# Kernel tuning notes

Hardware: AMD Instinct MI355X
Metric: run time of the kernel (lower is better)

## Reference

```python
import jax, jax.numpy as jnp
import numpy as np

B, S, D, K, N = 4, 4096, 768, 24, 8192

def setup_inputs() -> dict:
    key = jax.random.key(0)
    k1, k2, k3, k4 = jax.random.split(key, 4)
    x = jax.random.normal(k1, (B, S, D), dtype=jnp.float32)
    phi = jax.random.normal(k2, (S, K), dtype=jnp.float32)
    M_inputs = jax.random.normal(k3, (D, D), dtype=jnp.float32) / np.sqrt(D)
    M_filters = jax.random.normal(k4, (K, D), dtype=jnp.float32) / np.sqrt(K)
    return {"x": x, "phi": phi, "M_inputs": M_inputs, "M_filters": M_filters, "n": N}


def reference(x, phi, M_inputs, M_filters, n):
    # STU.forward with use_approx=True, use_flash_fft=False
    bsz, sl, d = x.shape
    x_proj = x @ M_inputs               # [B, S, D]
    phi_proj = phi @ M_filters          # [S, D]
    # alternating sign sequence for the 'minus' spectral branch
    sgn = jnp.ones((1, sl, 1), dtype=x.dtype).at[:, 1::2].set(-1.0)
    # filters: [1, S, D, 1] broadcast over the plus/minus stack
    v = phi_proj[None, :, :, None]
    V = jnp.fft.rfft(v, n=n, axis=1)    # [1, n//2+1, D, 1] complex
    U = jnp.stack([x_proj, x_proj * sgn], axis=-1)  # [B, S, D, 2]
    Uf = jnp.fft.rfft(U, n=n, axis=1)   # [B, n//2+1, D, 2]
    U_conv = jnp.fft.irfft(V * Uf, n=n, axis=1)[:, :sl]  # [B, S, D, 2]
    spectral_plus = U_conv[..., 0]
    spectral_minus = U_conv[..., 1] * sgn
    return spectral_plus + spectral_minus
```

## Files before the change

kernel.cpp:

```cpp
#include <hip/hip_runtime.h>
#include <hip/hip_bf16.h>


#define NB 4
#define NS 4096
#define ND 768
#define NK 24

typedef __attribute__((ext_vector_type(8))) short short8;
typedef __attribute__((ext_vector_type(4))) float f32x4;
typedef __attribute__((ext_vector_type(4))) unsigned short u16x4;

static __device__ __forceinline__ float bf2f(unsigned short u) {
  union { unsigned int i; float f; } v; v.i = ((unsigned int)u) << 16; return v.f;
}
static __device__ __forceinline__ unsigned short f2bf(float f) {
  union { float f; unsigned int i; } v; v.f = f;
  return (unsigned short)((v.i + 0x7fffu + ((v.i >> 16) & 1u)) >> 16);
}
static __device__ __forceinline__ unsigned int f2bf2(float lo, float hi) {
  unsigned int r;
  asm("v_cvt_pk_bf16_f32 %0, %1, %2" : "=v"(r) : "v"(lo), "v"(hi));
  return r;
}

__device__ __forceinline__ float2 cadd(float2 a, float2 b){ return make_float2(a.x+b.x, a.y+b.y); }
__device__ __forceinline__ float2 csub(float2 a, float2 b){ return make_float2(a.x-b.x, a.y-b.y); }
__device__ __forceinline__ float2 cmul(float2 a, float2 b){ return make_float2(a.x*b.x-a.y*b.y, a.x*b.y+a.y*b.x); }
__device__ __forceinline__ float2 cmulc(float2 a, float2 b){ return make_float2(a.x*b.x+a.y*b.y, a.y*b.x-a.x*b.y); }

#define C4 0.70710678118654752f
#define C8 0.92387953251128674f
#define S8 0.38268343236508977f
#define TWO_PI 6.28318530717958648f

__device__ __forceinline__ void fft16_dif(float2 v[16]) {
  const float twr[8] = {1.f, C8, C4, S8, 0.f, -S8, -C4, -C8};
  const float twi[8] = {0.f, -S8, -C4, -C8, -1.f, -C8, -C4, -S8};
#pragma unroll
  for (int i = 0; i < 8; ++i) {
    float2 a = v[i], b = v[i+8];
    v[i] = cadd(a, b);
    float2 d = csub(a, b);
    v[i+8] = make_float2(d.x*twr[i]-d.y*twi[i], d.x*twi[i]+d.y*twr[i]);
  }
#pragma unroll
  for (int blk = 0; blk < 16; blk += 8)
#pragma unroll
    for (int i = 0; i < 4; ++i) {
      float2 a = v[blk+i], b = v[blk+i+4];
      v[blk+i] = cadd(a, b);
      float2 d = csub(a, b);
      v[blk+i+4] = make_float2(d.x*twr[2*i]-d.y*twi[2*i], d.x*twi[2*i]+d.y*twr[2*i]);
    }
#pragma unroll
  for (int blk = 0; blk < 16; blk += 4) {
    { float2 a = v[blk],   b = v[blk+2]; v[blk] = cadd(a,b);   v[blk+2] = csub(a,b); }
    { float2 a = v[blk+1], b = v[blk+3]; float2 d = csub(a,b);
      v[blk+1] = cadd(a,b); v[blk+3] = make_float2(d.y, -d.x); }
  }
#pragma unroll
  for (int blk = 0; blk < 16; blk += 2) {
    float2 a = v[blk], b = v[blk+1];
    v[blk] = cadd(a, b); v[blk+1] = csub(a, b);
  }
}

__device__ __forceinline__ void fft16_dif_zero8(float2 v[16]) {
  const float twr[8] = {1.f, C8, C4, S8, 0.f, -S8, -C4, -C8};
  const float twi[8] = {0.f, -S8, -C4, -C8, -1.f, -C8, -C4, -S8};
#pragma unroll
  for (int i = 1; i < 8; ++i) {
    float2 a = v[i];
    v[i+8] = make_float2(a.x*twr[i]-a.y*twi[i], a.x*twi[i]+a.y*twr[i]);
  }
  v[8] = v[0];
#pragma unroll
  for (int blk = 0; blk < 16; blk += 8)
#pragma unroll
    for (int i = 0; i < 4; ++i) {
      float2 a = v[blk+i], b = v[blk+i+4];
      v[blk+i] = cadd(a, b);
      float2 d = csub(a, b);
      v[blk+i+4] = make_float2(d.x*twr[2*i]-d.y*twi[2*i], d.x*twi[2*i]+d.y*twr[2*i]);
    }
#pragma unroll
  for (int blk = 0; blk < 16; blk += 4) {
    { float2 a = v[blk],   b = v[blk+2]; v[blk] = cadd(a,b);   v[blk+2] = csub(a,b); }
    { float2 a = v[blk+1], b = v[blk+3]; float2 d = csub(a,b);
      v[blk+1] = cadd(a,b); v[blk+3] = make_float2(d.y, -d.x); }
  }
#pragma unroll
  for (int blk = 0; blk < 16; blk += 2) {
    float2 a = v[blk], b = v[blk+1];
    v[blk] = cadd(a, b); v[blk+1] = csub(a, b);
  }
}

__device__ __forceinline__ void idft16(float2 v[16]) {
  const float twr[8] = {1.f, C8, C4, S8, 0.f, -S8, -C4, -C8};
  const float twi[8] = {0.f, S8, C4, C8, 1.f, C8, C4, S8};
#pragma unroll
  for (int blk = 0; blk < 16; blk += 2) {
    float2 a = v[blk], b = v[blk+1];
    v[blk] = cadd(a, b); v[blk+1] = csub(a, b);
  }
#pragma unroll
  for (int blk = 0; blk < 16; blk += 4) {
    { float2 a = v[blk],   b = v[blk+2]; v[blk] = cadd(a,b);   v[blk+2] = csub(a,b); }
    { float2 a = v[blk+1], b = v[blk+3]; float2 t = make_float2(-b.y, b.x);
      v[blk+1] = cadd(a,t); v[blk+3] = csub(a,t); }
  }
#pragma unroll
  for (int blk = 0; blk < 16; blk += 8)
#pragma unroll
    for (int i = 0; i < 4; ++i) {
      float2 b = v[blk+i+4];
      float2 t = make_float2(b.x*twr[2*i]-b.y*twi[2*i], b.x*twi[2*i]+b.y*twr[2*i]);
      float2 a = v[blk+i];
      v[blk+i] = cadd(a, t); v[blk+i+4] = csub(a, t);
    }
#pragma unroll
  for (int i = 0; i < 8; ++i) {
    float2 b = v[i+8];
    float2 t = make_float2(b.x*twr[i]-b.y*twi[i], b.x*twi[i]+b.y*twr[i]);
    float2 a = v[i];
    v[i] = cadd(a, t); v[i+8] = csub(a, t);
  }
}

__device__ __forceinline__ void idft16_low8(float2 v[16]) {
  const float twr[8] = {1.f, C8, C4, S8, 0.f, -S8, -C4, -C8};
  const float twi[8] = {0.f, S8, C4, C8, 1.f, C8, C4, S8};
#pragma unroll
  for (int blk = 0; blk < 16; blk += 2) {
    float2 a = v[blk], b = v[blk+1];
    v[blk] = cadd(a, b); v[blk+1] = csub(a, b);
  }
#pragma unroll
  for (int blk = 0; blk < 16; blk += 4) {
    { float2 a = v[blk],   b = v[blk+2]; v[blk] = cadd(a,b);   v[blk+2] = csub(a,b); }
    { float2 a = v[blk+1], b = v[blk+3]; float2 t = make_float2(-b.y, b.x);
      v[blk+1] = cadd(a,t); v[blk+3] = csub(a,t); }
  }
#pragma unroll
  for (int blk = 0; blk < 16; blk += 8)
#pragma unroll
    for (int i = 0; i < 4; ++i) {
      float2 b = v[blk+i+4];
      float2 t = make_float2(b.x*twr[2*i]-b.y*twi[2*i], b.x*twi[2*i]+b.y*twr[2*i]);
      float2 a = v[blk+i];
      v[blk+i] = cadd(a, t); v[blk+i+4] = csub(a, t);
    }
#pragma unroll
  for (int i = 0; i < 8; ++i) {
    float2 b = v[i+8];
    float2 t = make_float2(b.x*twr[i]-b.y*twi[i], b.x*twi[i]+b.y*twr[i]);
    v[i] = cadd(v[i], t);
  }
}

#define BR_TABLE {0,8,4,12,2,10,6,14,1,9,5,13,3,11,7,15}
#define PAD(i) ((i) + ((i) >> 4))

__global__ __launch_bounds__(256) void transpose_cast_Mi(const float* __restrict__ Mi,
                                                         unsigned short* __restrict__ MiT) {
  __shared__ float tile[64][65];
  const int d0 = blockIdx.x * 64;
  const int e0 = blockIdx.y * 64;
  const int tid = threadIdx.x;
#pragma unroll
  for (int i = 0; i < 16; ++i) {
    int ee = (tid >> 6) + i * 4;
    int dd = tid & 63;
    tile[ee][dd] = Mi[(e0 + ee) * ND + d0 + dd];
  }
  __syncthreads();
#pragma unroll
  for (int i = 0; i < 8; ++i) {
    int dd = (tid >> 5) + i * 8;
    int ee2 = (tid & 31) * 2;
    unsigned int w = f2bf2(tile[ee2][dd], tile[ee2 + 1][dd]);
    *(unsigned int*)(MiT + (size_t)(d0 + dd) * ND + e0 + ee2) = w;
  }
}

__global__ __launch_bounds__(256) void gemm_xprojT(const float* __restrict__ Xf,
                                                   const unsigned short* __restrict__ MiT,
                                                   unsigned short* __restrict__ XPT) {
  __shared__ __align__(16) unsigned char smem[33792];
  unsigned short* As0 = (unsigned short*)smem;
  unsigned short* Bs0 = As0 + 4096;
  unsigned short* As1 = Bs0 + 4096;
  unsigned short* Bs1 = As1 + 4096;

  const int tid = threadIdx.x;
  const int lane = tid & 63;
  const int wave = tid >> 6;
  const int f = blockIdx.x;
  const int swz = (f & 7) * 96 + (f >> 3);
  const int c0 = (swz % 6) * 128;
  const int r0 = (swz / 6) * 128;

  const int rowA = tid >> 2;
  const int colq = (tid & 3) * 8;

  f32x4 acc[4][4];
#pragma unroll
  for (int m = 0; m < 4; ++m)
#pragma unroll
    for (int n = 0; n < 4; ++n) acc[m][n] = (f32x4){0.f, 0.f, 0.f, 0.f};

  {
    const float* ga = Xf + (size_t)(r0 + rowA) * ND + colq;
    float4 p0 = *(const float4*)ga, p1 = *(const float4*)(ga + 4);
    const float* ga2 = ga + (size_t)64 * ND;
    float4 p2 = *(const float4*)ga2, p3 = *(const float4*)(ga2 + 4);
#pragma unroll
    for (int h = 0; h < 2; ++h) {
      int c = wave * 2 + h;
      int rowc = c * 16 + (lane >> 2);
      const unsigned short* gb = MiT + (size_t)(c0 + rowc) * ND + (lane & 3) * 8;
      __builtin_amdgcn_global_load_lds(
          (const __attribute__((address_space(1))) void*)gb,
          (__attribute__((address_space(3))) void*)(Bs0 + c * 512), 16, 0, 0);
    }
    *(uint4*)(As0 + tid * 8) = make_uint4(
        f2bf2(p0.x, p0.y), f2bf2(p0.z, p0.w), f2bf2(p1.x, p1.y), f2bf2(p1.z, p1.w));
    *(uint4*)(As0 + 2048 + tid * 8) = make_uint4(
        f2bf2(p2.x, p2.y), f2bf2(p2.z, p2.w), f2bf2(p3.x, p3.y), f2bf2(p3.z, p3.w));
  }
  __syncthreads();

  for (int t = 0; t < NK; ++t) {
    unsigned short* Ac = (t & 1) ? As1 : As0;
    unsigned short* Bc = (t & 1) ? Bs1 : Bs0;
    unsigned short* An = (t & 1) ? As0 : As1;
    unsigned short* Bn = (t & 1) ? Bs0 : Bs1;
    const bool pre = (t < NK - 1);
    float4 p0, p1, p2, p3;
    if (pre) {
      const int k0n = (t + 1) * 32;
      const float* ga = Xf + (size_t)(r0 + rowA) * ND + k0n + colq;
      p0 = *(const float4*)ga; p1 = *(const float4*)(ga + 4);
      const float* ga2 = ga + (size_t)64 * ND;
      p2 = *(const float4*)ga2; p3 = *(const float4*)(ga2 + 4);
#pragma unroll
      for (int h = 0; h < 2; ++h) {
        int c = wave * 2 + h;
        int rowc = c * 16 + (lane >> 2);
        const unsigned short* gb = MiT + (size_t)(c0 + rowc) * ND + k0n + (lane & 3) * 8;
        __builtin_amdgcn_global_load_lds(
            (const __attribute__((address_space(1))) void*)gb,
            (__attribute__((address_space(3))) void*)(Bn + c * 512), 16, 0, 0);
      }
    }

    const int wr = (wave >> 1) * 64;
    const int wc = (wave & 1) * 64;
    short8 a[4], b[4];
#pragma unroll
    for (int m = 0; m < 4; ++m)
      a[m] = *(const short8*)(Ac + (wr + m * 16 + (lane & 15)) * 32 + (lane >> 4) * 8);
#pragma unroll
    for (int n = 0; n < 4; ++n)
      b[n] = *(const short8*)(Bc + (wc + n * 16 + (lane & 15)) * 32 + (lane >> 4) * 8);
#pragma unroll
    for (int m = 0; m < 4; ++m)
#pragma unroll
      for (int n = 0; n < 4; ++n)
        acc[m][n] = __builtin_amdgcn_mfma_f32_16x16x32_bf16(a[m], b[n], acc[m][n], 0, 0, 0);

    if (pre) {
      *(uint4*)(An + tid * 8) = make_uint4(
          f2bf2(p0.x, p0.y), f2bf2(p0.z, p0.w), f2bf2(p1.x, p1.y), f2bf2(p1.z, p1.w));
      *(uint4*)(An + 2048 + tid * 8) = make_uint4(
          f2bf2(p2.x, p2.y), f2bf2(p2.z, p2.w), f2bf2(p3.x, p3.y), f2bf2(p3.z, p3.w));
      __syncthreads();
    }
  }
  __syncthreads();

  unsigned int* Cb = (unsigned int*)smem;
  const int wr = (wave >> 1) * 64;
  const int wc = (wave & 1) * 64;
#pragma unroll
  for (int m = 0; m < 4; ++m)
#pragma unroll
    for (int n = 0; n < 4; ++n) {
      int col = wc + n * 16 + (lane & 15);
      int sp = (wr + m * 16 + (lane >> 4) * 4) >> 1;
      f32x4 a4 = acc[m][n];
      *(uint2*)(Cb + col * 66 + sp) =
          make_uint2(f2bf2(a4[0], a4[1]), f2bf2(a4[2], a4[3]));
    }
  __syncthreads();
  const int bI = r0 >> 12;
  const int sBase = r0 & (NS - 1);
  {
    int col = tid >> 1, half = tid & 1;
    const unsigned int* srcl = Cb + col * 66 + half * 32;
    unsigned int* dstg = (unsigned int*)(XPT + ((size_t)bI * ND + c0 + col) * NS + sBase) + half * 32;
#pragma unroll
    for (int k = 0; k < 8; ++k)
      *(uint4*)(dstg + k * 4) = *(const uint4*)(srcl + k * 4);
  }
}

__global__ __launch_bounds__(256) void filter_fft(const float* __restrict__ phi,
                                                  const float* __restrict__ Mf,
                                                  float2* __restrict__ Hbr) {
  __shared__ float LR[4352], LI[4352];
  __shared__ float2 TA[256], TB[256];
  const int d = blockIdx.x;
  const int tid = threadIdx.x;
  const int BR[16] = BR_TABLE;
  float2 v[16];

  {
    float sn, cs;
    __sincosf(-(TWO_PI / 4096.f) * (float)tid, &sn, &cs); TA[tid] = make_float2(cs, sn);
    __sincosf(-(TWO_PI / 256.f) * (float)tid, &sn, &cs);  TB[tid] = make_float2(cs, sn);
  }

  float mf[NK];
#pragma unroll
  for (int k = 0; k < NK; ++k) mf[k] = Mf[k * ND + d];
#pragma unroll
  for (int n2 = 0; n2 < 8; ++n2) {
    int m = n2 * 256 + tid;
    const float* pr = phi + (size_t)(2 * m) * NK;
    float acc = 0.f;
#pragma unroll
    for (int k = 0; k < NK; ++k) acc += pr[k] * mf[k];
    v[n2] = make_float2(acc, 0.f);
  }
#pragma unroll
  for (int n2 = 8; n2 < 16; ++n2) v[n2] = make_float2(0.f, 0.f);

  fft16_dif_zero8(v);
  __syncthreads();
  const int t1 = tid >> 4, t0 = tid & 15;
#pragma unroll
  for (int p = 1; p < 16; ++p) v[BR[p]] = cmul(v[BR[p]], cmul(TB[p * t1], TA[p * t0]));
#pragma unroll
  for (int r = 0; r < 16; ++r) { int i = BR[r] * 256 + tid; int s = PAD(i); LR[s] = v[r].x; LI[s] = v[r].y; }
  __syncthreads();

  const int p2 = tid >> 4, n0 = tid & 15;
#pragma unroll
  for (int n1 = 0; n1 < 16; ++n1) { int i = p2 * 256 + n1 * 16 + n0; int s = PAD(i); v[n1] = make_float2(LR[s], LI[s]); }
  fft16_dif(v);
#pragma unroll
  for (int p = 1; p < 16; ++p) v[BR[p]] = cmul(v[BR[p]], TB[p * n0]);
  __syncthreads();
#pragma unroll
  for (int r = 0; r < 16; ++r) { int i = p2 * 256 + BR[r] * 16 + n0; int s = PAD(i); LR[s] = v[r].x; LI[s] = v[r].y; }
  __syncthreads();

#pragma unroll
  for (int q = 0; q < 16; ++q) { int i = tid * 16 + q; int s = PAD(i); v[q] = make_float2(LR[s], LI[s]); }
  fft16_dif(v);
  const float sc = 2.0f / 4096.0f;
  float2* H = Hbr + (size_t)d * 4096;
#pragma unroll
  for (int r = 0; r < 16; ++r)
    H[r * 256 + tid] = make_float2(v[r].x * sc, v[r].y * sc);
}

__global__ __launch_bounds__(256) void conv_kernel(const unsigned short* __restrict__ XPT,
                                                   const float2* __restrict__ Hbr,
                                                   unsigned int* __restrict__ outTb) {
  __shared__ float LR[4352], LI[4352];
  __shared__ float2 TA[256], TB[256];
  const int bd = blockIdx.x;
  const int d = bd % ND;
  const int tid = threadIdx.x;
  const int BR[16] = BR_TABLE;
  float2 v[16];

  {
    float sn, cs;
    __sincosf(-(TWO_PI / 4096.f) * (float)tid, &sn, &cs); TA[tid] = make_float2(cs, sn);
    __sincosf(-(TWO_PI / 256.f) * (float)tid, &sn, &cs);  TB[tid] = make_float2(cs, sn);
  }

  const unsigned int* src = (const unsigned int*)(XPT + (size_t)bd * NS);
#pragma unroll
  for (int n2 = 0; n2 < 8; ++n2) {
    unsigned int w = src[n2 * 256 + tid];
    v[n2] = make_float2(bf2f((unsigned short)(w & 0xffffu)), bf2f((unsigned short)(w >> 16)));
  }
#pragma unroll
  for (int n2 = 8; n2 < 16; ++n2) v[n2] = make_float2(0.f, 0.f);

  fft16_dif_zero8(v);
  __syncthreads();
  const int t1 = tid >> 4, t0 = tid & 15;
#pragma unroll
  for (int p = 1; p < 16; ++p) v[BR[p]] = cmul(v[BR[p]], cmul(TB[p * t1], TA[p * t0]));
#pragma unroll
  for (int r = 0; r < 16; ++r) { int i = BR[r] * 256 + tid; int s = PAD(i); LR[s] = v[r].x; LI[s] = v[r].y; }
  __syncthreads();

  const int p2 = tid >> 4, n0 = tid & 15;
#pragma unroll
  for (int n1 = 0; n1 < 16; ++n1) { int i = p2 * 256 + n1 * 16 + n0; int s = PAD(i); v[n1] = make_float2(LR[s], LI[s]); }
  fft16_dif(v);
#pragma unroll
  for (int p = 1; p < 16; ++p) v[BR[p]] = cmul(v[BR[p]], TB[p * n0]);
  __syncthreads();
#pragma unroll
  for (int r = 0; r < 16; ++r) { int i = p2 * 256 + BR[r] * 16 + n0; int s = PAD(i); LR[s] = v[r].x; LI[s] = v[r].y; }
  __syncthreads();

#pragma unroll
  for (int q = 0; q < 16; ++q) { int i = tid * 16 + q; int s = PAD(i); v[q] = make_float2(LR[s], LI[s]); }
  fft16_dif(v);
  const float2* H = Hbr + (size_t)d * 4096;
#pragma unroll
  for (int r = 0; r < 16; ++r) v[r] = cmul(v[r], H[r * 256 + tid]);
  idft16(v);
#pragma unroll
  for (int n = 1; n < 16; ++n) v[n] = cmulc(v[n], TB[n * (tid & 15)]);
#pragma unroll
  for (int n = 0; n < 16; ++n) { int i = tid * 16 + n; int s = PAD(i); LR[s] = v[n].x; LI[s] = v[n].y; }
  __syncthreads();

#pragma unroll
  for (int r = 0; r < 16; ++r) { int i = p2 * 256 + BR[r] * 16 + n0; int s = PAD(i); v[r] = make_float2(LR[s], LI[s]); }
  idft16(v);
  {
    float2 cA = TA[p2 * n0];
#pragma unroll
    for (int n = 0; n < 16; ++n) v[n] = cmulc(v[n], cmul(TB[p2 * n], cA));
  }
  __syncthreads();
#pragma unroll
  for (int n = 0; n < 16; ++n) { int i = p2 * 256 + n * 16 + n0; int s = PAD(i); LR[s] = v[n].x; LI[s] = v[n].y; }
  __syncthreads();

#pragma unroll
  for (int r = 0; r < 16; ++r) { int i = BR[r] * 256 + tid; int s = PAD(i); v[r] = make_float2(LR[s], LI[s]); }
  idft16_low8(v);
  unsigned int* dst = outTb + (size_t)bd * 2048;
#pragma unroll
  for (int n2 = 0; n2 < 8; ++n2) {
    float2 y = v[n2];
    dst[(n2 << 8) + tid] = f2bf2(y.x, y.y);
  }
}

__global__ __launch_bounds__(256) void transpose_out(const unsigned int* __restrict__ outTb,
                                                     float* __restrict__ out) {
  __shared__ float tile[64][65];
  const int b = blockIdx.z;
  const int d0 = blockIdx.y * 64;
  const int s0 = blockIdx.x * 64;
  const int tid = threadIdx.x;
#pragma unroll
  for (int i = 0; i < 8; ++i) {
    int dd = (tid >> 5) + i * 8;
    int ss2 = (tid & 31) * 2;
    unsigned int w = outTb[(((size_t)b * ND + d0 + dd) * NS + s0 + ss2) >> 1];
    tile[dd][ss2]     = bf2f((unsigned short)(w & 0xffffu));
    tile[dd][ss2 + 1] = bf2f((unsigned short)(w >> 16));
  }
  __syncthreads();
#pragma unroll
  for (int i = 0; i < 16; ++i) {
    int ss = (tid >> 6) + i * 4;
    int dd = tid & 63;
    out[((size_t)b * NS + s0 + ss) * ND + d0 + dd] = tile[dd][ss];
  }
}

extern "C" void kernel_launch(void* const* d_in, const int* in_sizes, int n_in,
                              void* d_out, int out_size, void* d_ws, size_t ws_size,
                              hipStream_t stream) {
  const float* x   = (const float*)d_in[0];
  const float* phi = (const float*)d_in[1];
  const float* Mi  = (const float*)d_in[2];
  const float* Mf  = (const float*)d_in[3];
  float* out = (float*)d_out;

  const size_t SZ_XPT = (size_t)NB * ND * NS * 2;
  const size_t SZ_HBR = (size_t)ND * 4096 * 8;
  const size_t SZ_POOL = (size_t)NB * ND * NS * 4;
  if (ws_size < SZ_XPT + SZ_HBR + SZ_POOL) return;

  char* ws = (char*)d_ws;
  unsigned short* xprojT = (unsigned short*)ws;
  float2* Hbr = (float2*)(ws + SZ_XPT);
  char* pool = ws + SZ_XPT + SZ_HBR;
  unsigned int* outTb = (unsigned int*)pool;
  unsigned short* MiT = (unsigned short*)(pool + 25165824);

  transpose_cast_Mi<<<dim3(ND / 64, ND / 64), 256, 0, stream>>>(Mi, MiT);
  gemm_xprojT<<<768, 256, 0, stream>>>(x, MiT, xprojT);
  filter_fft<<<ND, 256, 0, stream>>>(phi, Mf, Hbr);
  conv_kernel<<<NB * ND, 256, 0, stream>>>(xprojT, Hbr, outTb);
  transpose_out<<<dim3(NS / 64, ND / 64, NB), 256, 0, stream>>>(outTb, out);
}
```

Baseline: 121.9 us.

## Software-pipeline x-projection GEMM with two-ahead A prefetch and manual waitcnt

Restructures the gemm_xprojT main loop into an unrolled-by-two software pipeline. The fp32 A tile is prefetched two K-steps ahead into alternating register sets, and sched_barrier plus explicit vmcnt/lgkmcnt waits pin the order of global loads, MFMA compute and LDS packing. The aim is to hide global memory latency behind the MFMAs and to avoid the compiler's conservative full waits. In exchange it holds more live registers and depends on hand-counted wait values, which are easy to get wrong.

```diff
diff --git a/kernel.cpp b/kernel.cpp
--- a/kernel.cpp
+++ b/kernel.cpp
@@ -184,6 +184,54 @@
     *(unsigned int*)(MiT + (size_t)(d0 + dd) * ND + e0 + ee2) = w;
   }
 }
+
+#define G_ISSUE_B(BUFB, T)                                                     \
+  {                                                                            \
+    const int k0n = (T) * 32;                                                  \
+    _Pragma("unroll")                                                          \
+    for (int h = 0; h < 2; ++h) {                                              \
+      int c = wave * 2 + h;                                                    \
+      int rowc = c * 16 + (lane >> 2);                                         \
+      const unsigned short* gb = MiT + (size_t)(c0 + rowc) * ND + k0n + (lane & 3) * 8; \
+      __builtin_amdgcn_global_load_lds(                                        \
+          (const __attribute__((address_space(1))) void*)gb,                   \
+          (__attribute__((address_space(3))) void*)((BUFB) + c * 512), 16, 0, 0); \
+    }                                                                          \
+  }
+
+#define G_LOAD_A(REG, T)                                                       \
+  {                                                                            \
+    const float* ga = Xf + (size_t)(r0 + rowA) * ND + (T) * 32 + colq;         \
+    REG[0] = *(const float4*)ga; REG[1] = *(const float4*)(ga + 4);            \
+    const float* ga2 = ga + (size_t)64 * ND;                                   \
+    REG[2] = *(const float4*)ga2; REG[3] = *(const float4*)(ga2 + 4);          \
+  }
+
+#define G_PACK(BUFA, REG)                                                      \
+  {                                                                            \
+    *(uint4*)((BUFA) + tid * 8) = make_uint4(                                  \
+        f2bf2(REG[0].x, REG[0].y), f2bf2(REG[0].z, REG[0].w),                  \
+        f2bf2(REG[1].x, REG[1].y), f2bf2(REG[1].z, REG[1].w));                 \
+    *(uint4*)((BUFA) + 2048 + tid * 8) = make_uint4(                           \
+        f2bf2(REG[2].x, REG[2].y), f2bf2(REG[2].z, REG[2].w),                  \
+        f2bf2(REG[3].x, REG[3].y), f2bf2(REG[3].z, REG[3].w));                 \
+  }
+
+#define G_COMP(BUFA, BUFB)                                                     \
+  {                                                                            \
+    short8 a[4], b[4];                                                         \
+    _Pragma("unroll")                                                          \
+    for (int m = 0; m < 4; ++m)                                                \
+      a[m] = *(const short8*)((BUFA) + (wr + m * 16 + (lane & 15)) * 32 + (lane >> 4) * 8); \
+    _Pragma("unroll")                                                          \
+    for (int n = 0; n < 4; ++n)                                                \
+      b[n] = *(const short8*)((BUFB) + (wc + n * 16 + (lane & 15)) * 32 + (lane >> 4) * 8); \
+    _Pragma("unroll")                                                          \
+    for (int m = 0; m < 4; ++m)                                                \
+      _Pragma("unroll")                                                        \
+      for (int n = 0; n < 4; ++n)                                              \
+        acc[m][n] = __builtin_amdgcn_mfma_f32_16x16x32_bf16(a[m], b[n], acc[m][n], 0, 0, 0); \
+  }
 
 __global__ __launch_bounds__(256) void gemm_xprojT(const float* __restrict__ Xf,
                                                    const unsigned short* __restrict__ MiT,
@@ -204,86 +252,66 @@
 
   const int rowA = tid >> 2;
   const int colq = (tid & 3) * 8;
-
-  f32x4 acc[4][4];
-#pragma unroll
-  for (int m = 0; m < 4; ++m)
-#pragma unroll
-    for (int n = 0; n < 4; ++n) acc[m][n] = (f32x4){0.f, 0.f, 0.f, 0.f};
-
-  {
-    const float* ga = Xf + (size_t)(r0 + rowA) * ND + colq;
-    float4 p0 = *(const float4*)ga, p1 = *(const float4*)(ga + 4);
-    const float* ga2 = ga + (size_t)64 * ND;
-    float4 p2 = *(const float4*)ga2, p3 = *(const float4*)(ga2 + 4);
-#pragma unroll
-    for (int h = 0; h < 2; ++h) {
-      int c = wave * 2 + h;
-      int rowc = c * 16 + (lane >> 2);
-      const unsigned short* gb = MiT + (size_t)(c0 + rowc) * ND + (lane & 3) * 8;
-      __builtin_amdgcn_global_load_lds(
-          (const __attribute__((address_space(1))) void*)gb,
-          (__attribute__((address_space(3))) void*)(Bs0 + c * 512), 16, 0, 0);
-    }
-    *(uint4*)(As0 + tid * 8) = make_uint4(
-        f2bf2(p0.x, p0.y), f2bf2(p0.z, p0.w), f2bf2(p1.x, p1.y), f2bf2(p1.z, p1.w));
-    *(uint4*)(As0 + 2048 + tid * 8) = make_uint4(
-        f2bf2(p2.x, p2.y), f2bf2(p2.z, p2.w), f2bf2(p3.x, p3.y), f2bf2(p3.z, p3.w));
-  }
-  __syncthreads();
-
-  for (int t = 0; t < NK; ++t) {
-    unsigned short* Ac = (t & 1) ? As1 : As0;
-    unsigned short* Bc = (t & 1) ? Bs1 : Bs0;
-    unsigned short* An = (t & 1) ? As0 : As1;
-    unsigned short* Bn = (t & 1) ? Bs0 : Bs1;
-    const bool pre = (t < NK - 1);
-    float4 p0, p1, p2, p3;
-    if (pre) {
-      const int k0n = (t + 1) * 32;
-      const float* ga = Xf + (size_t)(r0 + rowA) * ND + k0n + colq;
-      p0 = *(const float4*)ga; p1 = *(const float4*)(ga + 4);
-      const float* ga2 = ga + (size_t)64 * ND;
-      p2 = *(const float4*)ga2; p3 = *(const float4*)(ga2 + 4);
-#pragma unroll
-      for (int h = 0; h < 2; ++h) {
-        int c = wave * 2 + h;
-        int rowc = c * 16 + (lane >> 2);
-        const unsigned short* gb = MiT + (size_t)(c0 + rowc) * ND + k0n + (lane & 3) * 8;
-        __builtin_amdgcn_global_load_lds(
-            (const __attribute__((address_space(1))) void*)gb,
-            (__attribute__((address_space(3))) void*)(Bn + c * 512), 16, 0, 0);
-      }
-    }
-
-    const int wr = (wave >> 1) * 64;
-    const int wc = (wave & 1) * 64;
-    short8 a[4], b[4];
-#pragma unroll
-    for (int m = 0; m < 4; ++m)
-      a[m] = *(const short8*)(Ac + (wr + m * 16 + (lane & 15)) * 32 + (lane >> 4) * 8);
-#pragma unroll
-    for (int n = 0; n < 4; ++n)
-      b[n] = *(const short8*)(Bc + (wc + n * 16 + (lane & 15)) * 32 + (lane >> 4) * 8);
-#pragma unroll
-    for (int m = 0; m < 4; ++m)
-#pragma unroll
-      for (int n = 0; n < 4; ++n)
-        acc[m][n] = __builtin_amdgcn_mfma_f32_16x16x32_bf16(a[m], b[n], acc[m][n], 0, 0, 0);
-
-    if (pre) {
-      *(uint4*)(An + tid * 8) = make_uint4(
-          f2bf2(p0.x, p0.y), f2bf2(p0.z, p0.w), f2bf2(p1.x, p1.y), f2bf2(p1.z, p1.w));
-      *(uint4*)(An + 2048 + tid * 8) = make_uint4(
-          f2bf2(p2.x, p2.y), f2bf2(p2.z, p2.w), f2bf2(p3.x, p3.y), f2bf2(p3.z, p3.w));
-      __syncthreads();
-    }
-  }
-  __syncthreads();
-
-  unsigned int* Cb = (unsigned int*)smem;
   const int wr = (wave >> 1) * 64;
   const int wc = (wave & 1) * 64;
+
+  f32x4 acc[4][4];
+#pragma unroll
+  for (int m = 0; m < 4; ++m)
+#pragma unroll
+    for (int n = 0; n < 4; ++n) acc[m][n] = (f32x4){0.f, 0.f, 0.f, 0.f};
+
+  float4 pA[4], pB[4];
+
+  G_ISSUE_B(Bs0, 0);
+  __builtin_amdgcn_sched_barrier(0);
+  G_LOAD_A(pA, 0);
+  G_PACK(As0, pA);
+  G_LOAD_A(pB, 1);
+  __builtin_amdgcn_sched_barrier(0);
+  asm volatile("s_waitcnt lgkmcnt(0)" ::: "memory");
+  __builtin_amdgcn_s_barrier();
+  __builtin_amdgcn_sched_barrier(0);
+
+  for (int tt = 0; tt < 22; tt += 2) {
+    G_ISSUE_B(Bs1, tt + 1);
+    __builtin_amdgcn_sched_barrier(0);
+    G_LOAD_A(pA, tt + 2);
+    __builtin_amdgcn_sched_barrier(0);
+    G_COMP(As0, Bs0);
+    G_PACK(As1, pB);
+    __builtin_amdgcn_sched_barrier(0);
+    asm volatile("s_waitcnt vmcnt(4)" ::: "memory");
+    asm volatile("s_waitcnt lgkmcnt(0)" ::: "memory");
+    __builtin_amdgcn_s_barrier();
+    __builtin_amdgcn_sched_barrier(0);
+
+    G_ISSUE_B(Bs0, tt + 2);
+    __builtin_amdgcn_sched_barrier(0);
+    G_LOAD_A(pB, tt + 3);
+    __builtin_amdgcn_sched_barrier(0);
+    G_COMP(As1, Bs1);
+    G_PACK(As0, pA);
+    __builtin_amdgcn_sched_barrier(0);
+    asm volatile("s_waitcnt vmcnt(4)" ::: "memory");
+    asm volatile("s_waitcnt lgkmcnt(0)" ::: "memory");
+    __builtin_amdgcn_s_barrier();
+    __builtin_amdgcn_sched_barrier(0);
+  }
+  G_ISSUE_B(Bs1, 23);
+  __builtin_amdgcn_sched_barrier(0);
+  G_COMP(As0, Bs0);
+  G_PACK(As1, pB);
+  __builtin_amdgcn_sched_barrier(0);
+  asm volatile("s_waitcnt vmcnt(0)" ::: "memory");
+  asm volatile("s_waitcnt lgkmcnt(0)" ::: "memory");
+  __builtin_amdgcn_s_barrier();
+  __builtin_amdgcn_sched_barrier(0);
+  G_COMP(As1, Bs1);
+
+  __syncthreads();
+
+  unsigned int* Cb = (unsigned int*)smem;
 #pragma unroll
   for (int m = 0; m < 4; ++m)
 #pragma unroll
```

New measurement: 130.2 us. +6.8%, slower.
